# Optimization experiments

Measured on AMD Instinct MI355X. Metric: run time of the kernel, lower is better.

## Reference

```python
import jax, jax.numpy as jnp
import numpy as np

NUM_HEADS = 16
ROPE_BASE = 10000.0


def _rope(x):
    # x: (B, T, H, D); torchtune-style interleaved rotary embedding
    B, T, H, D = x.shape
    inv_freq = 1.0 / (ROPE_BASE ** (jnp.arange(0, D, 2, dtype=jnp.float32) / D))  # (D/2,)
    ang = jnp.arange(T, dtype=jnp.float32)[:, None] * inv_freq[None, :]  # (T, D/2)
    cos = jnp.cos(ang)[None, :, None, :].astype(x.dtype)  # (1,T,1,D/2)
    sin = jnp.sin(ang)[None, :, None, :].astype(x.dtype)
    x1 = x[..., 0::2]
    x2 = x[..., 1::2]
    r1 = x1 * cos - x2 * sin
    r2 = x2 * cos + x1 * sin
    return jnp.stack([r1, r2], axis=-1).reshape(B, T, H, D)


def _attention(x, Wq, Wk, Wv, Wo, bo):
    B, T, C = x.shape
    H = NUM_HEADS
    D = C // H
    q = (x @ Wq).reshape(B, T, H, D)
    k = (x @ Wk).reshape(B, T, H, D)
    v = (x @ Wv).reshape(B, T, H, D)
    q = _rope(q)
    k = _rope(k)
    # (B, H, T, D)
    q = q.transpose(0, 2, 1, 3)
    k = k.transpose(0, 2, 1, 3)
    v = v.transpose(0, 2, 1, 3)
    scale = 1.0 / jnp.sqrt(jnp.asarray(D, dtype=x.dtype))
    scores = jnp.einsum('bhqd,bhkd->bhqk', q, k) * scale  # (B,H,T,T)
    causal = jnp.tril(jnp.ones((T, T), dtype=bool))
    scores = jnp.where(causal[None, None, :, :], scores, jnp.asarray(-jnp.inf, dtype=scores.dtype))
    attn = jax.nn.softmax(scores, axis=-1)
    out = jnp.einsum('bhqk,bhkd->bhqd', attn, v)  # (B,H,T,D)
    out = out.transpose(0, 2, 1, 3).reshape(B, T, C)
    return out @ Wo + bo  # dropout is identity in eval mode


def setup_inputs() -> dict:
    key = jax.random.key(0)
    ks = jax.random.split(key, 6)
    B, T, C = 2, 2048, 1024
    s = 1.0 / np.sqrt(C)
    return {
        'x': jax.random.normal(ks[0], (B, T, C), dtype=jnp.float32),
        'Wq': jax.random.normal(ks[1], (C, C), dtype=jnp.float32) * s,
        'Wk': jax.random.normal(ks[2], (C, C), dtype=jnp.float32) * s,
        'Wv': jax.random.normal(ks[3], (C, C), dtype=jnp.float32) * s,
        'Wo': jax.random.normal(ks[4], (C, C), dtype=jnp.float32) * s,
        'bo': jnp.zeros((C,), dtype=jnp.float32),
    }


def reference(x, Wq, Wk, Wv, Wo, bo):
    return _attention(x, Wq, Wk, Wv, Wo, bo)
```

## Files before the change

### kernel.cpp

```cpp
#include <hip/hip_runtime.h>
#include <stdint.h>

#define BATCH 2
#define T_SEQ 2048
#define CDIM  1024
#define NH    16
#define HD    64
#define MROWS (BATCH*T_SEQ)

typedef unsigned short u16;
typedef __attribute__((ext_vector_type(8))) short bf16x8;
typedef __attribute__((ext_vector_type(4))) float f32x4;
typedef __attribute__((ext_vector_type(16))) float f32x16;
typedef __attribute__((ext_vector_type(4))) unsigned short u16x4;

__constant__ int qc_tab[40] = {0,1,2,3, 4,4,5,5,6,6,7,7,
                               8,8,8,9,9,9,10,10,10,11,11,11,
                               12,12,12,12,13,13,13,13,14,14,14,14,15,15,15,15};
__constant__ int ck_tab[40] = {0,0,0,0, 0,1,0,1,0,1,0,1,
                               0,1,2,0,1,2,0,1,2,0,1,2,
                               0,1,2,3,0,1,2,3,0,1,2,3,0,1,2,3};
__constant__ int base_tab[16] = {0,1,2,3,4,6,8,10,12,15,18,21,24,28,32,36};
__constant__ int nch_tab[16]  = {1,1,1,1,2,2,2,2,3,3,3,3,4,4,4,4};

__device__ __forceinline__ u16 f2b(float f) {
  union { float f; unsigned int u; } x; x.f = f;
  unsigned int r = x.u + 0x7FFFu + ((x.u >> 16) & 1u);
  return (u16)(r >> 16);
}

__device__ __forceinline__ float b2f(u16 b) {
  union { unsigned int u; float f; } x; x.u = ((unsigned int)b) << 16;
  return x.f;
}

__device__ __forceinline__ float fexp2(float x) {
  float r;
  asm("v_exp_f32 %0, %1" : "=v"(r) : "v"(x));
  return r;
}

__device__ __forceinline__ void gload16(const void* g, void* s) {
  __builtin_amdgcn_global_load_lds(
      (const __attribute__((address_space(1))) void*)g,
      (__attribute__((address_space(3))) void*)s, 16, 0, 0);
}

__device__ __forceinline__ int cvtpk(float lo, float hi_) {
  int w;
  asm("v_cvt_pk_bf16_f32 %0, %1, %2" : "=v"(w) : "v"(lo), "v"(hi_));
  return w;
}

__device__ __forceinline__ bf16x8 mkfrag(int a, int b, int c, int d) {
  union { int i[4]; bf16x8 v; } u;
  u.i[0] = a; u.i[1] = b; u.i[2] = c; u.i[3] = d;
  return u.v;
}

__global__ __launch_bounds__(256) void cvt4(const float4* __restrict__ in,
                                            u16x4* __restrict__ out, int n4) {
  int i = blockIdx.x * 256 + threadIdx.x;
  if (i < n4) {
    float4 v = in[i];
    u16x4 o = { f2b(v.x), f2b(v.y), f2b(v.z), f2b(v.w) };
    out[i] = o;
  }
}

__global__ __launch_bounds__(256) void w_trans4(const float* __restrict__ W0,
                                                const float* __restrict__ W1,
                                                const float* __restrict__ W2,
                                                const float* __restrict__ W3,
                                                u16* __restrict__ D0,
                                                u16* __restrict__ D3) {
  __shared__ u16 tile[64][72];
  const float* W = (blockIdx.z == 0) ? W0 : (blockIdx.z == 1) ? W1
                 : (blockIdx.z == 2) ? W2 : W3;
  u16* Wt = (blockIdx.z == 3) ? D3 : (D0 + (size_t)blockIdx.z * CDIM * CDIM);
  int k0 = blockIdx.x * 64, n0 = blockIdx.y * 64;
  int tid = threadIdx.x;
  #pragma unroll
  for (int i = 0; i < 16; ++i) {
    int c = i * 256 + tid;
    int kr = c >> 6, nc = c & 63;
    tile[kr][nc] = f2b(W[(size_t)(k0 + kr) * CDIM + n0 + nc]);
  }
  __syncthreads();
  #pragma unroll
  for (int i = 0; i < 16; ++i) {
    int c = i * 256 + tid;
    int nr = c >> 6, kc = c & 63;
    Wt[(size_t)(n0 + nr) * CDIM + k0 + kc] = tile[kc][nr];
  }
}

__global__ __launch_bounds__(256) void rope_tab(float* __restrict__ cosT,
                                                float* __restrict__ sinT) {
  int i = blockIdx.x * 256 + threadIdx.x;
  int t = i >> 5, j = i & 31;
  float inv = expf(-(float)j * (9.210340371976184f / 32.0f));
  float ang = (float)t * inv;
  cosT[i] = cosf(ang);
  sinT[i] = sinf(ang);
}

__global__ __launch_bounds__(512, 2) void gemm_qkv256(const u16* __restrict__ A,
                                                      const u16* __restrict__ Bt,
                                                      const float* __restrict__ cosT,
                                                      const float* __restrict__ sinT,
                                                      u16* __restrict__ Qr,
                                                      u16* __restrict__ Kr,
                                                      u16* __restrict__ Vt) {
  __shared__ __align__(16) char smem[114688];
  const int tid = threadIdx.x;
  const int wid = tid >> 6, lane = tid & 63;
  const int wm = wid >> 2, wn = wid & 3;
  const int col = lane & 15, kq = lane >> 4;
  const int xcd = blockIdx.x & 7, bi = blockIdx.x >> 3;
  const int arow0 = (bi & 15) * 256;
  const int bcol0 = (xcd * 2 + (bi >> 4)) * 192;

  auto STAGE = [&](int k0, int bsel) {
    char* dA = smem + bsel * 57344;
    char* dB = dA + 32768;
    #pragma unroll
    for (int i = 0; i < 4; ++i) {
      int idx = i * 512 + tid;
      int r = idx >> 3, p = idx & 7;
      int src = (p ^ (r & 7)) << 3;
      gload16(A + (size_t)(arow0 + r) * CDIM + k0 + src, dA + idx * 16);
    }
    #pragma unroll
    for (int i = 0; i < 3; ++i) {
      int idx = i * 512 + tid;
      int r = idx >> 3, p = idx & 7;
      int src = (p ^ (r & 7)) << 3;
      gload16(Bt + (size_t)(bcol0 + r) * CDIM + k0 + src, dB + idx * 16);
    }
  };

  f32x4 acc[8][3] = {};

  STAGE(0, 0);
  for (int kt = 0; kt < 16; ++kt) {
    if (kt < 15) {
      STAGE((kt + 1) * 64, (kt + 1) & 1);
      asm volatile("s_waitcnt vmcnt(7)" ::: "memory");
    } else {
      asm volatile("s_waitcnt vmcnt(0)" ::: "memory");
    }
    __builtin_amdgcn_s_barrier();

    const char* As_ = smem + (kt & 1) * 57344;
    const char* Bs_ = As_ + 32768;

    bf16x8 bfr[3][2];
    #pragma unroll
    for (int n = 0; n < 3; ++n)
      #pragma unroll
      for (int ks = 0; ks < 2; ++ks) {
        int rowb = wn * 48 + n * 16 + col;
        bfr[n][ks] = *(const bf16x8*)(Bs_ + rowb * 128 + (((ks * 4 + kq) ^ (rowb & 7)) << 4));
      }

    #pragma unroll
    for (int p = 0; p < 4; ++p) {
      bf16x8 ap[2][2];
      #pragma unroll
      for (int mm = 0; mm < 2; ++mm)
        #pragma unroll
        for (int ks = 0; ks < 2; ++ks) {
          int row = wm * 128 + (p * 2 + mm) * 16 + col;
          ap[mm][ks] = *(const bf16x8*)(As_ + row * 128 + (((ks * 4 + kq) ^ (row & 7)) << 4));
        }
      __builtin_amdgcn_s_setprio(1);
      #pragma unroll
      for (int mm = 0; mm < 2; ++mm)
        #pragma unroll
        for (int n = 0; n < 3; ++n)
          #pragma unroll
          for (int ks = 0; ks < 2; ++ks)
            acc[p * 2 + mm][n] = __builtin_amdgcn_mfma_f32_16x16x32_bf16(
                ap[mm][ks], bfr[n][ks], acc[p * 2 + mm][n], 0, 0, 0);
      __builtin_amdgcn_s_setprio(0);
      __builtin_amdgcn_s_barrier();
    }
  }

  #pragma unroll
  for (int im = 0; im < 8; ++im)
    #pragma unroll
    for (int in = 0; in < 3; ++in) {
      int cc = bcol0 + wn * 48 + in * 16 + col;
      int type = cc >> 10;
      int cm = cc & 1023;
      int h = cm >> 6, d = cm & 63;
      int rr0 = arow0 + wm * 128 + im * 16 + kq * 4;
      if (type == 2) {
        int b = rr0 >> 11, t = rr0 & 2047;
        u16x4 v4 = { f2b(acc[im][in][0]), f2b(acc[im][in][1]),
                     f2b(acc[im][in][2]), f2b(acc[im][in][3]) };
        *(u16x4*)(Vt + (((size_t)(b * NH + h)) * 64 + d) * T_SEQ + t) = v4;
      } else {
        int j = d >> 1;
        u16* dst = type ? Kr : Qr;
        #pragma unroll
        for (int i = 0; i < 4; ++i) {
          int rr = rr0 + i;
          int b = rr >> 11, t = rr & 2047;
          float val = acc[im][in][i];
          float pv = __shfl_xor(val, 1, 64);
          float c = cosT[t * 32 + j], s = sinT[t * 32 + j];
          float r = (d & 1) ? (val * c + pv * s) : (val * c - pv * s);
          if (type == 0) r *= 0.18033688011112042f;
          dst[(((size_t)(b * NH + h)) * T_SEQ + t) * 64 + d] = f2b(r);
        }
      }
    }
}

__global__ __launch_bounds__(256, 2) void gemm_bt(const u16* __restrict__ A,
                                                  const u16* __restrict__ Bt,
                                                  float* __restrict__ C,
                                                  const float* __restrict__ bias,
                                                  int K, int ldc) {
  __shared__ __align__(16) char smem[65536];
  const int tid = threadIdx.x;
  const int wid = tid >> 6, lane = tid & 63;
  const int wr = wid >> 1, wc = wid & 1;
  const int col = lane & 15, kq = lane >> 4;
  const int swz = (blockIdx.x & 7) * 32 + (blockIdx.x >> 3);
  const int arow0 = (swz & 31) * 128, bcol0 = (swz >> 5) * 128;
  const int NT = K >> 6;

  auto STAGE = [&](int k0, int bsel) {
    char* dA = smem + bsel * 32768;
    char* dB = dA + 16384;
    #pragma unroll
    for (int i = 0; i < 4; ++i) {
      int idx = i * 256 + tid;
      int r = idx >> 3, p = idx & 7;
      int src = (p ^ (r & 7)) << 3;
      gload16(A  + (size_t)(arow0 + r) * K + k0 + src, dA + idx * 16);
      gload16(Bt + (size_t)(bcol0 + r) * K + k0 + src, dB + idx * 16);
    }
  };

  f32x4 acc[4][4] = {};

  STAGE(0, 0);
  for (int kt = 0; kt < NT; ++kt) {
    if (kt + 1 < NT) {
      STAGE((kt + 1) * 64, (kt + 1) & 1);
      asm volatile("s_waitcnt vmcnt(8)" ::: "memory");
    } else {
      asm volatile("s_waitcnt vmcnt(0)" ::: "memory");
    }
    __builtin_amdgcn_s_barrier();
    const char* As_ = smem + (kt & 1) * 32768;
    const char* Bs_ = As_ + 16384;
    bf16x8 a[4][2], b[4][2];
    #pragma unroll
    for (int m = 0; m < 4; ++m)
      #pragma unroll
      for (int ks = 0; ks < 2; ++ks) {
        int row = wr * 64 + m * 16 + col;
        a[m][ks] = *(const bf16x8*)(As_ + row * 128 + (((ks * 4 + kq) ^ (row & 7)) << 4));
      }
    #pragma unroll
    for (int n = 0; n < 4; ++n)
      #pragma unroll
      for (int ks = 0; ks < 2; ++ks) {
        int rowb = wc * 64 + n * 16 + col;
        b[n][ks] = *(const bf16x8*)(Bs_ + rowb * 128 + (((ks * 4 + kq) ^ (rowb & 7)) << 4));
      }
    __builtin_amdgcn_s_setprio(1);
    #pragma unroll
    for (int m = 0; m < 4; ++m)
      #pragma unroll
      for (int n = 0; n < 4; ++n)
        #pragma unroll
        for (int ks = 0; ks < 2; ++ks)
          acc[m][n] = __builtin_amdgcn_mfma_f32_16x16x32_bf16(a[m][ks], b[n][ks],
                                                              acc[m][n], 0, 0, 0);
    __builtin_amdgcn_s_setprio(0);
    __builtin_amdgcn_s_barrier();
  }

  #pragma unroll
  for (int m = 0; m < 4; ++m)
    #pragma unroll
    for (int n = 0; n < 4; ++n) {
      int cc = bcol0 + wc * 64 + n * 16 + col;
      float bv = bias ? bias[cc] : 0.0f;
      #pragma unroll
      for (int i = 0; i < 4; ++i) {
        int rr = arow0 + wr * 64 + m * 16 + kq * 4 + i;
        C[(size_t)rr * ldc + cc] = acc[m][n][i] + bv;
      }
    }
}

__global__ __launch_bounds__(256, 4) void attn_fwd8(const u16* __restrict__ Q,
                                                    const u16* __restrict__ K,
                                                    const u16* __restrict__ V,
                                                    u16* __restrict__ OP,
                                                    float* __restrict__ LP) {
  __shared__ __align__(16) char smem[32768];

  const int bh = blockIdx.x;
  const int w = 39 - blockIdx.y;
  const int qc = qc_tab[w], ck = ck_tab[w];
  const int q0 = qc << 7;
  const int nkt = 2 * (qc + 1);
  const int start = ck * 8;
  const int end = min(start + 8, nkt);
  const int slot = w * 32 + bh;

  const int tid = threadIdx.x;
  const int wid = tid >> 6, lane = tid & 63;
  const int l31 = lane & 31, hi = lane >> 5;
  const int wq0 = q0 + wid * 32;
  const int qrow = wq0 + l31;

  bf16x8 qa[4];
  const u16* qbase = Q + ((size_t)bh * T_SEQ + qrow) * 64 + hi * 8;
  #pragma unroll
  for (int dk = 0; dk < 4; ++dk)
    qa[dk] = *(const bf16x8*)(qbase + dk * 16);

  const u16* kb = K + (size_t)bh * T_SEQ * 64;
  const u16* vb = V + (size_t)bh * 64 * T_SEQ;

  auto STAGE = [&](int kt, int bsel) {
    char* dstK = smem + bsel * 16384;
    char* dstV = dstK + 8192;
    int kv0 = kt << 6;
    #pragma unroll
    for (int i = 0; i < 2; ++i) {
      int idx = i * 256 + tid;
      int r = idx >> 3, c = idx & 7;
      int cs = (c ^ (r & 7)) << 3;
      gload16(kb + (size_t)(kv0 + r) * 64 + cs, dstK + idx * 16);
      gload16(vb + (size_t)r * T_SEQ + kv0 + cs, dstV + idx * 16);
    }
  };

  float L = 0.f;
  f32x16 ot0 = {}, ot1 = {};
  const int swl = (l31 & 7);

  STAGE(start, 0);

  for (int kt = start; kt < end; ++kt) {
    const int kv0 = kt << 6;
    const int cur = (kt - start) & 1;
    asm volatile("s_waitcnt vmcnt(0)" ::: "memory");
    __builtin_amdgcn_s_barrier();
    if (kt + 1 < end) STAGE(kt + 1, cur ^ 1);

    if (kv0 <= wq0 + 31) {
      const char* Ks = smem + cur * 16384;
      const char* Vs = Ks + 8192;

      f32x16 st0 = {}, st1 = {};
      __builtin_amdgcn_s_setprio(1);
      #pragma unroll
      for (int dk = 0; dk < 4; ++dk) {
        int ch = dk * 2 + hi;
        bf16x8 ka0 = *(const bf16x8*)(Ks + l31 * 128 + ((ch ^ swl) << 4));
        bf16x8 ka1 = *(const bf16x8*)(Ks + (l31 + 32) * 128 + ((ch ^ swl) << 4));
        st0 = __builtin_amdgcn_mfma_f32_32x32x16_bf16(ka0, qa[dk], st0, 0, 0, 0);
        st1 = __builtin_amdgcn_mfma_f32_32x32x16_bf16(ka1, qa[dk], st1, 0, 0, 0);
      }
      __builtin_amdgcn_s_setprio(0);

      if (kv0 + 63 > wq0) {
        #pragma unroll
        for (int r = 0; r < 16; ++r) {
          int kl = (r & 3) + 8 * (r >> 2) + 4 * hi;
          if (kv0 + kl > qrow)      st0[r] = -1e30f;
          if (kv0 + 32 + kl > qrow) st1[r] = -1e30f;
        }
      }

      float s0 = 0.f, s1 = 0.f, s2 = 0.f, s3 = 0.f;
      #pragma unroll
      for (int r = 0; r < 16; r += 4) {
        st0[r]     = fexp2(st0[r]);     st1[r]     = fexp2(st1[r]);
        st0[r + 1] = fexp2(st0[r + 1]); st1[r + 1] = fexp2(st1[r + 1]);
        st0[r + 2] = fexp2(st0[r + 2]); st1[r + 2] = fexp2(st1[r + 2]);
        st0[r + 3] = fexp2(st0[r + 3]); st1[r + 3] = fexp2(st1[r + 3]);
        s0 += st0[r]     + st1[r];
        s1 += st0[r + 1] + st1[r + 1];
        s2 += st0[r + 2] + st1[r + 2];
        s3 += st0[r + 3] + st1[r + 3];
      }
      float sum = (s0 + s1) + (s2 + s3);
      sum += __shfl_xor(sum, 32, 64);
      L += sum;

      int x0 = cvtpk(st0[0], st0[1]),   y0 = cvtpk(st0[4], st0[5]);
      int x1 = cvtpk(st0[2], st0[3]),   y1 = cvtpk(st0[6], st0[7]);
      int x2 = cvtpk(st0[8], st0[9]),   y2 = cvtpk(st0[12], st0[13]);
      int x3 = cvtpk(st0[10], st0[11]), y3 = cvtpk(st0[14], st0[15]);
      asm("v_permlane32_swap_b32 %0, %1" : "+v"(x0), "+v"(y0));
      asm("v_permlane32_swap_b32 %0, %1" : "+v"(x1), "+v"(y1));
      asm("v_permlane32_swap_b32 %0, %1" : "+v"(x2), "+v"(y2));
      asm("v_permlane32_swap_b32 %0, %1" : "+v"(x3), "+v"(y3));
      int z0 = cvtpk(st1[0], st1[1]),   w0 = cvtpk(st1[4], st1[5]);
      int z1 = cvtpk(st1[2], st1[3]),   w1 = cvtpk(st1[6], st1[7]);
      int z2 = cvtpk(st1[8], st1[9]),   w2 = cvtpk(st1[12], st1[13]);
      int z3 = cvtpk(st1[10], st1[11]), w3 = cvtpk(st1[14], st1[15]);
      asm("v_permlane32_swap_b32 %0, %1" : "+v"(z0), "+v"(w0));
      asm("v_permlane32_swap_b32 %0, %1" : "+v"(z1), "+v"(w1));
      asm("v_permlane32_swap_b32 %0, %1" : "+v"(z2), "+v"(w2));
      asm("v_permlane32_swap_b32 %0, %1" : "+v"(z3), "+v"(w3));
      bf16x8 pb[4];
      pb[0] = mkfrag(x0, x1, y0, y1);
      pb[1] = mkfrag(x2, x3, y2, y3);
      pb[2] = mkfrag(z0, z1, w0, w1);
      pb[3] = mkfrag(z2, z3, w2, w3);

      __builtin_amdgcn_s_setprio(1);
      #pragma unroll
      for (int ks = 0; ks < 4; ++ks) {
        int ch = ks * 2 + hi;
        bf16x8 va0 = *(const bf16x8*)(Vs + l31 * 128 + ((ch ^ swl) << 4));
        bf16x8 va1 = *(const bf16x8*)(Vs + (l31 + 32) * 128 + ((ch ^ swl) << 4));
        ot0 = __builtin_amdgcn_mfma_f32_32x32x16_bf16(va0, pb[ks], ot0, 0, 0, 0);
        ot1 = __builtin_amdgcn_mfma_f32_32x32x16_bf16(va1, pb[ks], ot1, 0, 0, 0);
      }
      __builtin_amdgcn_s_setprio(0);
    }
  }

  u16* op = OP + (size_t)slot * 8192;
  const int qloc = wid * 32 + l31;
  #pragma unroll
  for (int r = 0; r < 16; ++r) {
    int d_ = (r & 3) + 8 * (r >> 2) + 4 * hi;
    op[d_ * 128 + qloc]        = f2b(ot0[r]);
    op[(32 + d_) * 128 + qloc] = f2b(ot1[r]);
  }
  if (hi == 0) LP[(size_t)slot * 128 + qloc] = L;
}

__global__ __launch_bounds__(256) void attn_comb(const u16* __restrict__ OP,
                                                 const float* __restrict__ LP,
                                                 u16* __restrict__ Ob) {
  __shared__ float tr[64 * 132];
  const int qc = blockIdx.x, head = blockIdx.y;
  const int nch = nch_tab[qc], base = base_tab[qc];
  const int tid = threadIdx.x;

  {
    int d = tid >> 2, q4 = (tid & 3) * 32;
    float a[32];
    #pragma unroll
    for (int j = 0; j < 32; ++j) a[j] = 0.f;
    for (int c = 0; c < nch; ++c) {
      const u16* p = OP + ((size_t)((base + c) * 32 + head)) * 8192 + d * 128 + q4;
      #pragma unroll
      for (int jv = 0; jv < 4; ++jv) {
        bf16x8 v = *(const bf16x8*)(p + jv * 8);
        #pragma unroll
        for (int j = 0; j < 8; ++j)
          a[jv * 8 + j] += b2f((u16)v[j]);
      }
    }
    #pragma unroll
    for (int j = 0; j < 32; ++j) tr[d * 132 + q4 + j] = a[j];
  }
  __syncthreads();

  int q = tid >> 1, d0 = (tid & 1) * 32;
  float Lt = 0.f;
  for (int c = 0; c < nch; ++c)
    Lt += LP[((size_t)((base + c) * 32 + head)) * 128 + q];
  float inv = 1.0f / Lt;

  int outw[16];
  #pragma unroll
  for (int j = 0; j < 16; ++j) {
    float lo  = tr[(d0 + 2 * j) * 132 + q] * inv;
    float hi_ = tr[(d0 + 2 * j + 1) * 132 + q] * inv;
    outw[j] = cvtpk(lo, hi_);
  }
  int b = head >> 4, h = head & 15;
  size_t row = (size_t)(b * T_SEQ + qc * 128 + q);
  int* dst = (int*)(Ob + row * 1024 + h * 64 + d0);
  #pragma unroll
  for (int j = 0; j < 4; ++j) {
    int4 v = { outw[j * 4], outw[j * 4 + 1], outw[j * 4 + 2], outw[j * 4 + 3] };
    *(int4*)(dst + j * 4) = v;
  }
}

extern "C" void kernel_launch(void* const* d_in, const int* in_sizes, int n_in,
                              void* d_out, int out_size, void* d_ws, size_t ws_size,
                              hipStream_t stream) {
  (void)in_sizes; (void)n_in; (void)out_size; (void)ws_size;
  const float* x  = (const float*)d_in[0];
  const float* Wq = (const float*)d_in[1];
  const float* Wk = (const float*)d_in[2];
  const float* Wv = (const float*)d_in[3];
  const float* Wo = (const float*)d_in[4];
  const float* bo = (const float*)d_in[5];
  float* out = (float*)d_out;

  char* ws = (char*)d_ws;
  u16*   xb   = (u16*)(ws);
  u16*   Wqkv = (u16*)(ws + (size_t)( 8u << 20));
  u16*   Wot  = (u16*)(ws + (size_t)(14u << 20));
  u16*   Qr   = (u16*)(ws + (size_t)(16u << 20));
  u16*   Kr   = (u16*)(ws + (size_t)(24u << 20));
  u16*   Vt   = (u16*)(ws + (size_t)(32u << 20));
  u16*   Ob   = (u16*)(ws + (size_t)(40u << 20));
  float* cosT = (float*)(ws + (size_t)(48u << 20));
  float* sinT = (float*)(ws + (size_t)(48u << 20) + (1u << 18));
  u16*   OP   = (u16*)(ws + (size_t)(49u << 20));
  float* LP   = (float*)(ws + (size_t)(89u << 20));

  cvt4<<<dim3(MROWS * CDIM / 4 / 256), dim3(256), 0, stream>>>(
      (const float4*)x, (u16x4*)xb, MROWS * CDIM / 4);
  w_trans4<<<dim3(16, 16, 4), dim3(256), 0, stream>>>(Wq, Wk, Wv, Wo, Wqkv, Wot);
  rope_tab<<<dim3(T_SEQ * 32 / 256), dim3(256), 0, stream>>>(cosT, sinT);

  gemm_qkv256<<<dim3(256), dim3(512), 0, stream>>>(xb, Wqkv, cosT, sinT, Qr, Kr, Vt);

  attn_fwd8<<<dim3(32, 40), dim3(256), 0, stream>>>(Qr, Kr, Vt, OP, LP);
  attn_comb<<<dim3(16, 32), dim3(256), 0, stream>>>(OP, LP, Ob);

  gemm_bt<<<dim3(256), dim3(256), 0, stream>>>(Ob, Wot, out, bo, CDIM, CDIM);
}
```

Baseline: 105.4 us.

## Widen attention blocks to 256 query rows with 8 waves sharing K/V tiles

The attention kernel now uses 512-thread blocks covering 256 query rows per head (8 waves), so each staged K/V tile in shared memory feeds twice as many query rows. The causal work split is rebalanced with new start/end tables giving uneven KV-chunk ranges per split, and the combine kernel indexes the wider partial buffers by half. The aim is to halve K/V global loads per query and cut block count. The cost is fewer blocks (640) with coarser causal granularity, plus a launch bound of 8 that may constrain registers per wave.

```diff
diff --git a/kernel.cpp b/kernel.cpp
--- a/kernel.cpp
+++ b/kernel.cpp
@@ -14,14 +14,11 @@
 typedef __attribute__((ext_vector_type(16))) float f32x16;
 typedef __attribute__((ext_vector_type(4))) unsigned short u16x4;
 
-__constant__ int qc_tab[40] = {0,1,2,3, 4,4,5,5,6,6,7,7,
-                               8,8,8,9,9,9,10,10,10,11,11,11,
-                               12,12,12,12,13,13,13,13,14,14,14,14,15,15,15,15};
-__constant__ int ck_tab[40] = {0,0,0,0, 0,1,0,1,0,1,0,1,
-                               0,1,2,0,1,2,0,1,2,0,1,2,
-                               0,1,2,3,0,1,2,3,0,1,2,3,0,1,2,3};
-__constant__ int base_tab[16] = {0,1,2,3,4,6,8,10,12,15,18,21,24,28,32,36};
-__constant__ int nch_tab[16]  = {1,1,1,1,2,2,2,2,3,3,3,3,4,4,4,4};
+__constant__ int qc_tab[20] = {0, 1, 2,2, 3,3, 4,4,4, 5,5,5, 6,6,6,6, 7,7,7,7};
+__constant__ int st_tab[20] = {0, 0, 0,6, 0,8, 0,7,14, 0,8,16, 0,7,14,21, 0,8,16,24};
+__constant__ int en_tab[20] = {4, 8, 6,12, 8,16, 7,14,20, 8,16,24, 7,14,21,28, 8,16,24,32};
+__constant__ int base_tab[8] = {0,1,2,4,6,9,12,16};
+__constant__ int nch_tab[8]  = {1,1,2,2,3,3,4,4};
 
 __device__ __forceinline__ u16 f2b(float f) {
   union { float f; unsigned int u; } x; x.f = f;
@@ -302,20 +299,19 @@
     }
 }
 
-__global__ __launch_bounds__(256, 4) void attn_fwd8(const u16* __restrict__ Q,
-                                                    const u16* __restrict__ K,
-                                                    const u16* __restrict__ V,
-                                                    u16* __restrict__ OP,
-                                                    float* __restrict__ LP) {
+__global__ __launch_bounds__(512, 8) void attn_fwd11(const u16* __restrict__ Q,
+                                                     const u16* __restrict__ K,
+                                                     const u16* __restrict__ V,
+                                                     u16* __restrict__ OP,
+                                                     float* __restrict__ LP) {
   __shared__ __align__(16) char smem[32768];
 
   const int bh = blockIdx.x;
-  const int w = 39 - blockIdx.y;
-  const int qc = qc_tab[w], ck = ck_tab[w];
-  const int q0 = qc << 7;
-  const int nkt = 2 * (qc + 1);
-  const int start = ck * 8;
-  const int end = min(start + 8, nkt);
+  const int w = 19 - blockIdx.y;
+  const int qc = qc_tab[w];
+  const int q0 = qc << 8;
+  const int start = st_tab[w];
+  const int end = en_tab[w];
   const int slot = w * 32 + bh;
 
   const int tid = threadIdx.x;
@@ -337,14 +333,10 @@
     char* dstK = smem + bsel * 16384;
     char* dstV = dstK + 8192;
     int kv0 = kt << 6;
-    #pragma unroll
-    for (int i = 0; i < 2; ++i) {
-      int idx = i * 256 + tid;
-      int r = idx >> 3, c = idx & 7;
-      int cs = (c ^ (r & 7)) << 3;
-      gload16(kb + (size_t)(kv0 + r) * 64 + cs, dstK + idx * 16);
-      gload16(vb + (size_t)r * T_SEQ + kv0 + cs, dstV + idx * 16);
-    }
+    int r = tid >> 3, c = tid & 7;
+    int cs = (c ^ (r & 7)) << 3;
+    gload16(kb + (size_t)(kv0 + r) * 64 + cs, dstK + tid * 16);
+    gload16(vb + (size_t)r * T_SEQ + kv0 + cs, dstV + tid * 16);
   };
 
   float L = 0.f;
@@ -436,22 +428,23 @@
     }
   }
 
-  u16* op = OP + (size_t)slot * 8192;
+  u16* op = OP + (size_t)slot * 16384;
   const int qloc = wid * 32 + l31;
   #pragma unroll
   for (int r = 0; r < 16; ++r) {
     int d_ = (r & 3) + 8 * (r >> 2) + 4 * hi;
-    op[d_ * 128 + qloc]        = f2b(ot0[r]);
-    op[(32 + d_) * 128 + qloc] = f2b(ot1[r]);
-  }
-  if (hi == 0) LP[(size_t)slot * 128 + qloc] = L;
+    op[d_ * 256 + qloc]        = f2b(ot0[r]);
+    op[(32 + d_) * 256 + qloc] = f2b(ot1[r]);
+  }
+  if (hi == 0) LP[(size_t)slot * 256 + qloc] = L;
 }
 
 __global__ __launch_bounds__(256) void attn_comb(const u16* __restrict__ OP,
                                                  const float* __restrict__ LP,
                                                  u16* __restrict__ Ob) {
   __shared__ float tr[64 * 132];
-  const int qc = blockIdx.x, head = blockIdx.y;
+  const int qc = blockIdx.x >> 1, half = blockIdx.x & 1;
+  const int head = blockIdx.y;
   const int nch = nch_tab[qc], base = base_tab[qc];
   const int tid = threadIdx.x;
 
@@ -461,7 +454,8 @@
     #pragma unroll
     for (int j = 0; j < 32; ++j) a[j] = 0.f;
     for (int c = 0; c < nch; ++c) {
-      const u16* p = OP + ((size_t)((base + c) * 32 + head)) * 8192 + d * 128 + q4;
+      const u16* p = OP + ((size_t)((base + c) * 32 + head)) * 16384
+                     + d * 256 + half * 128 + q4;
       #pragma unroll
       for (int jv = 0; jv < 4; ++jv) {
         bf16x8 v = *(const bf16x8*)(p + jv * 8);
@@ -478,7 +472,7 @@
   int q = tid >> 1, d0 = (tid & 1) * 32;
   float Lt = 0.f;
   for (int c = 0; c < nch; ++c)
-    Lt += LP[((size_t)((base + c) * 32 + head)) * 128 + q];
+    Lt += LP[((size_t)((base + c) * 32 + head)) * 256 + half * 128 + q];
   float inv = 1.0f / Lt;
 
   int outw[16];
@@ -489,7 +483,7 @@
     outw[j] = cvtpk(lo, hi_);
   }
   int b = head >> 4, h = head & 15;
-  size_t row = (size_t)(b * T_SEQ + qc * 128 + q);
+  size_t row = (size_t)(b * T_SEQ + qc * 256 + half * 128 + q);
   int* dst = (int*)(Ob + row * 1024 + h * 64 + d0);
   #pragma unroll
   for (int j = 0; j < 4; ++j) {
@@ -530,7 +524,7 @@
 
   gemm_qkv256<<<dim3(256), dim3(512), 0, stream>>>(xb, Wqkv, cosT, sinT, Qr, Kr, Vt);
 
-  attn_fwd8<<<dim3(32, 40), dim3(256), 0, stream>>>(Qr, Kr, Vt, OP, LP);
+  attn_fwd11<<<dim3(32, 20), dim3(512), 0, stream>>>(Qr, Kr, Vt, OP, LP);
   attn_comb<<<dim3(16, 32), dim3(256), 0, stream>>>(OP, LP, Ob);
 
   gemm_bt<<<dim3(256), dim3(256), 0, stream>>>(Ob, Wot, out, bo, CDIM, CDIM);
```

After: 241.6 us. +129.1%, slower.
